# Optimization experiments

Measured on AMD Instinct MI355X. Metric: run time of the kernel, lower is better.

Reference implementation:

```python
import jax, jax.numpy as jnp
import numpy as np

N = 100000  # num nodes
E = 1600000  # num edges


def gcn_conv(x, edge_index, W, b):
    """PyG-style GCNConv: add self-loops, symmetric deg^-1/2 normalization,
    message = norm * (x @ W) gathered from src, scatter-add to dst, then + bias."""
    n = x.shape[0]
    loop = jnp.arange(n)
    src = jnp.concatenate([edge_index[0], loop])
    dst = jnp.concatenate([edge_index[1], loop])
    deg = jax.ops.segment_sum(jnp.ones_like(dst, dtype=x.dtype), dst, num_segments=n)
    dinv = jnp.where(deg > 0, jax.lax.rsqrt(deg), jnp.zeros_like(deg))
    norm = dinv[src] * dinv[dst]  # [E+N]
    h = x @ W  # dense transform first (out_dim <= in_dim here)
    msg = h[src] * norm[:, None]  # gather + scale, [E+N, out]
    out = jax.ops.segment_sum(msg, dst, num_segments=n)  # scatter-add
    return out + b


def setup_inputs() -> dict:
    key = jax.random.key(0)
    ks = jax.random.split(key, 6)
    x = jax.random.normal(ks[0], (N, 165), dtype=jnp.float32)
    edge_index = jax.random.randint(ks[1], (2, E), 0, N, dtype=jnp.int64)
    W1 = jax.random.normal(ks[2], (165, 128), dtype=jnp.float32) * 0.05
    b1 = jnp.zeros((128,), dtype=jnp.float32)
    W2 = jax.random.normal(ks[3], (128, 2), dtype=jnp.float32) * 0.05
    b2 = jnp.zeros((2,), dtype=jnp.float32)
    Ws = jax.random.normal(ks[4], (165, 2), dtype=jnp.float32) * 0.05
    bs = jnp.zeros((2,), dtype=jnp.float32)
    return {"x": x, "edge_index": edge_index, "W1": W1, "b1": b1,
            "W2": W2, "b2": b2, "Ws": Ws, "bs": bs}


def reference(x, edge_index, W1, b1, W2, b2, Ws, bs):
    h = jax.nn.relu(gcn_conv(x, edge_index, W1, b1))
    # dropout is identity at inference (training=False)
    out = gcn_conv(h, edge_index, W2, b2)
    return out + (x @ Ws + bs)
```

## Files before the change

kernel.cpp:

```cpp
#include <hip/hip_runtime.h>
#include <hip/hip_bf16.h>


#define IND 165
#define HID 128
#define KP 192
#define BM 32
#define XSS2 208
#define SLAB 8192
#define MAXNB 512

typedef __attribute__((ext_vector_type(8))) short short8v;
typedef __attribute__((ext_vector_type(4))) float float4v;
typedef __attribute__((ext_vector_type(2))) float float2v;

__device__ __forceinline__ unsigned short f2bf(float f) {
    unsigned u = __float_as_uint(f);
    unsigned r = (u + 0x7FFF + ((u >> 16) & 1)) >> 16;
    return (unsigned short)r;
}
__device__ __forceinline__ float bf2f(unsigned short s) { return __uint_as_float(((unsigned)s) << 16); }

__global__ __launch_bounds__(256) void setup_kernel(const float* __restrict__ W1,
                                                    unsigned short* __restrict__ w1t,
                                                    const int* __restrict__ e32,
                                                    int* __restrict__ flag,
                                                    int* __restrict__ bucket_len, int NB) {
    int b = blockIdx.x;
    if (b < 96) {
        int t = b * 256 + threadIdx.x;
        int nn = t / KP, k = t - nn * KP;
        w1t[t] = (k < IND) ? f2bf(W1[k * HID + nn]) : (unsigned short)0;
    } else {
        __shared__ int nz;
        if (threadIdx.x == 0) nz = 0;
        __syncthreads();
        if (e32[2 * threadIdx.x + 1] != 0) atomicOr(&nz, 1);
        __syncthreads();
        if (threadIdx.x == 0) flag[0] = (nz == 0) ? 1 : 0;
        for (int t = threadIdx.x; t < NB; t += 256) bucket_len[t] = 0;
    }
}

__global__ __launch_bounds__(256) void partition_kernel(const int* __restrict__ e32,
                                                        const int* __restrict__ flag,
                                                        int* __restrict__ bucket_len,
                                                        unsigned* __restrict__ slab,
                                                        int E, int NB) {
    __shared__ unsigned hist[MAXNB];
    __shared__ unsigned runbase[MAXNB];
    __shared__ unsigned cnt2[MAXNB];
    for (int t = threadIdx.x; t < NB; t += 256) { hist[t] = 0; cnt2[t] = 0; }
    __syncthreads();
    const int f = flag[0];
    const int base = blockIdx.x * 8192;
    unsigned rec[32];
    unsigned bk[32];
    #pragma unroll
    for (int j = 0; j < 32; ++j) {
        int e = base + j * 256 + threadIdx.x;
        if (e < E) {
            int src, dst;
            if (f) {
                int2 s2 = ((const int2*)e32)[e];
                int2 d2 = ((const int2*)e32)[E + e];
                src = s2.x; dst = d2.x;
            } else {
                src = e32[e];
                dst = e32[E + e];
            }
            unsigned b = (unsigned)dst >> 8;
            rec[j] = ((unsigned)(dst & 255) << 24) | (unsigned)src;
            bk[j] = b;
            atomicAdd(&hist[b], 1u);
        } else {
            bk[j] = 0xFFFFFFFFu;
            rec[j] = 0;
        }
    }
    __syncthreads();
    for (int t = threadIdx.x; t < NB; t += 256) {
        unsigned h = hist[t];
        runbase[t] = h ? (unsigned)atomicAdd(&bucket_len[t], (int)h) : 0u;
    }
    __syncthreads();
    #pragma unroll
    for (int j = 0; j < 32; ++j) {
        unsigned b = bk[j];
        if (b != 0xFFFFFFFFu) {
            unsigned p = runbase[b] + atomicAdd(&cnt2[b], 1u);
            if (p < SLAB) slab[(size_t)b * SLAB + p] = rec[j];
        }
    }
}

__global__ __launch_bounds__(256) void buildb_kernel(const unsigned* __restrict__ slab,
                                                     const int* __restrict__ bucket_len,
                                                     int2* __restrict__ row2,
                                                     float* __restrict__ dinv,
                                                     int* __restrict__ col_src, int n) {
    __shared__ unsigned deg[256];
    __shared__ int qa[256], qb[256];
    __shared__ unsigned cur[256];
    const int b = blockIdx.x;
    const int t = threadIdx.x;
    const int len = min(bucket_len[b], SLAB);
    const unsigned* recs = slab + (size_t)b * SLAB;
    const int d0 = b << 8;
    const int base = b * SLAB;
    deg[t] = 0;
    __syncthreads();
    for (int i = t; i < len; i += 256) atomicAdd(&deg[recs[i] >> 24], 1u);
    __syncthreads();
    const unsigned dv = deg[t];
    const int pdv = (int)((dv + 7u) & ~7u);
    qa[t] = pdv;
    __syncthreads();
    int* s = qa; int* d = qb;
    for (int off = 1; off < 256; off <<= 1) {
        d[t] = s[t] + ((t >= off) ? s[t - off] : 0);
        __syncthreads();
        int* tmp = s; s = d; d = tmp;
    }
    int pexcl = s[t] - pdv;
    int pend = min(pexcl + pdv, SLAB);
    if (pexcl > SLAB) pexcl = SLAB;
    if (d0 + t < n) {
        dinv[d0 + t] = rsqrtf(1.0f + (float)dv);
        row2[d0 + t] = make_int2(base + pexcl, base + pend);
    }
    cur[t] = (unsigned)pexcl;
    __syncthreads();
    for (int i = t; i < len; i += 256) {
        unsigned r = recs[i];
        unsigned p = atomicAdd(&cur[r >> 24], 1u);
        if (p < (unsigned)SLAB) col_src[base + p] = (int)(r & 0xFFFFFFu);
    }
    for (int p = pexcl + (int)dv; p < pend; ++p)
        col_src[base + p] = n;
}

__global__ __launch_bounds__(256, 4) void gemm1_kernel(const float* __restrict__ x,
                                                       const unsigned short* __restrict__ w1t,
                                                       const float* __restrict__ Ws,
                                                       const float* __restrict__ bs,
                                                       const float* __restrict__ b2,
                                                       const float* __restrict__ dinv,
                                                       unsigned char* __restrict__ hb8,
                                                       float* __restrict__ h2p,
                                                       float* __restrict__ skip, int n) {
    __shared__ unsigned short xs[BM * XSS2];
    __shared__ float sdinv[BM];
    const int row0 = blockIdx.x * BM;
    const int tid = threadIdx.x;
    const int wave = tid >> 6, lane = tid & 63;
    const int l15 = lane & 15, lk = (lane >> 4) * 8;

    if (blockIdx.x == 0) {
        if (tid < 32) ((unsigned*)(hb8 + (size_t)n * HID))[tid] = 0u;
        if (tid == 32) ((float2*)h2p)[n] = make_float2(0.f, 0.f);
    }
    if (tid < BM) sdinv[tid] = (row0 + tid < n) ? dinv[row0 + tid] : 1.f;

    short8v bfr[12];
    #pragma unroll
    for (int nt2 = 0; nt2 < 2; ++nt2)
        #pragma unroll
        for (int ks = 0; ks < 6; ++ks)
            bfr[nt2 * 6 + ks] =
                *(const short8v*)(w1t + (size_t)((2 * wave + nt2) * 16 + l15) * KP + ks * 32 + lk);

    for (int t = tid; t < BM * (XSS2 - IND); t += 256) {
        int r = t / (XSS2 - IND), k = IND + (t - r * (XSS2 - IND));
        xs[r * XSS2 + k] = 0;
    }
    {
        const int rows = min(BM, n - row0);
        const int nflt = rows * IND;
        const float2* xsrc = (const float2*)(x + (size_t)row0 * IND);
        const int nf2 = nflt >> 1;
        for (int f = tid; f < nf2; f += 256) {
            float2 v = xsrc[f];
            int e0 = 2 * f;
            int r0 = e0 / IND, k0 = e0 - r0 * IND;
            xs[r0 * XSS2 + k0] = f2bf(v.x);
            int r1 = (k0 == IND - 1) ? r0 + 1 : r0;
            int k1 = (k0 == IND - 1) ? 0 : k0 + 1;
            xs[r1 * XSS2 + k1] = f2bf(v.y);
        }
        if ((nflt & 1) && tid == 0) {
            int e = nflt - 1;
            int r = e / IND, k = e - r * IND;
            xs[r * XSS2 + k] = f2bf(x[(size_t)row0 * IND + e]);
        }
    }
    __syncthreads();

    float4v acc[2][2];
    #pragma unroll
    for (int m = 0; m < 2; ++m)
        #pragma unroll
        for (int nt2 = 0; nt2 < 2; ++nt2) acc[m][nt2] = (float4v){0.f, 0.f, 0.f, 0.f};
    #pragma unroll
    for (int m = 0; m < 2; ++m) {
        const unsigned short* arow = xs + (m * 16 + l15) * XSS2;
        #pragma unroll
        for (int ks = 0; ks < 6; ++ks) {
            short8v a = *(const short8v*)(arow + ks * 32 + lk);
            acc[m][0] = __builtin_amdgcn_mfma_f32_16x16x32_bf16(a, bfr[ks], acc[m][0], 0, 0, 0);
            acc[m][1] = __builtin_amdgcn_mfma_f32_16x16x32_bf16(a, bfr[6 + ks], acc[m][1], 0, 0, 0);
        }
    }

    #pragma unroll
    for (int m = 0; m < 2; ++m) {
        int rib0 = m * 16 + (lane >> 4) * 4;
        #pragma unroll
        for (int nt2 = 0; nt2 < 2; ++nt2) {
            int col = (2 * wave + nt2) * 16 + l15;
            #pragma unroll
            for (int r = 0; r < 4; ++r) {
                int row = row0 + rib0 + r;
                float hv = acc[m][nt2][r] * sdinv[rib0 + r];
                int pk = __builtin_amdgcn_cvt_pk_fp8_f32(hv, 0.f, 0, false);
                if (row < n) hb8[(size_t)row * HID + col] = (unsigned char)(pk & 0xFF);
            }
        }
    }

    {
        int r = tid >> 3, j = tid & 7;
        int row = row0 + r;
        float s0 = 0.f, s1 = 0.f;
        if (row < n) {
            const float2* Wsv = (const float2*)Ws;
            const unsigned short* xr = xs + r * XSS2;
            for (int k = j; k < IND; k += 8) {
                float xv = bf2f(xr[k]);
                float2 w = Wsv[k];
                s0 = fmaf(xv, w.x, s0);
                s1 = fmaf(xv, w.y, s1);
            }
        }
        s0 += __shfl_xor(s0, 1); s0 += __shfl_xor(s0, 2); s0 += __shfl_xor(s0, 4);
        s1 += __shfl_xor(s1, 1); s1 += __shfl_xor(s1, 2); s1 += __shfl_xor(s1, 4);
        if (j == 0 && row < n)
            ((float2*)skip)[row] = make_float2(s0 + bs[0] + b2[0], s1 + bs[1] + b2[1]);
    }
}

__global__ __launch_bounds__(256) void agg1_kernel(const unsigned char* __restrict__ hb8,
                                                   const float* __restrict__ dinv,
                                                   const int2* __restrict__ row2,
                                                   const int* __restrict__ col_src,
                                                   const float* __restrict__ b1,
                                                   const float* __restrict__ W2,
                                                   float* __restrict__ h2p, int n) {
    int wid = threadIdx.x >> 6, lane = threadIdx.x & 63;
    int i = blockIdx.x * 4 + wid;
    if (i >= n) return;
    const int slot = lane >> 4, cl = lane & 15;
    const float di = dinv[i];
    float2v a0, a1, a2, a3;
    {
        uint2 r = *(const uint2*)(hb8 + (size_t)i * 128 + cl * 8);
        float w = (slot == 0) ? 1.f : 0.f;
        float2v wv = {w, w};
        a0 = __builtin_amdgcn_cvt_pk_f32_fp8((int)r.x, false) * wv;
        a1 = __builtin_amdgcn_cvt_pk_f32_fp8((int)r.x, true)  * wv;
        a2 = __builtin_amdgcn_cvt_pk_f32_fp8((int)r.y, false) * wv;
        a3 = __builtin_amdgcn_cvt_pk_f32_fp8((int)r.y, true)  * wv;
    }
    const int2 be = row2[i];
    const int beg  = __builtin_amdgcn_readfirstlane(be.x);
    const int endv = __builtin_amdgcn_readfirstlane(be.y);
    for (int e = beg; e < endv; e += 8) {
        int4 c0 = *(const int4*)(col_src + e);
        int4 c1 = *(const int4*)(col_src + e + 4);
        int sx0 = (slot & 1) ? c0.y : c0.x;
        int sy0 = (slot & 1) ? c0.w : c0.z;
        int s0  = (slot & 2) ? sy0 : sx0;
        int sx1 = (slot & 1) ? c1.y : c1.x;
        int sy1 = (slot & 1) ? c1.w : c1.z;
        int s1  = (slot & 2) ? sy1 : sx1;
        uint2 r0 = *(const uint2*)(hb8 + (size_t)s0 * 128 + cl * 8);
        uint2 r1 = *(const uint2*)(hb8 + (size_t)s1 * 128 + cl * 8);
        a0 += __builtin_amdgcn_cvt_pk_f32_fp8((int)r0.x, false);
        a1 += __builtin_amdgcn_cvt_pk_f32_fp8((int)r0.x, true);
        a2 += __builtin_amdgcn_cvt_pk_f32_fp8((int)r0.y, false);
        a3 += __builtin_amdgcn_cvt_pk_f32_fp8((int)r0.y, true);
        a0 += __builtin_amdgcn_cvt_pk_f32_fp8((int)r1.x, false);
        a1 += __builtin_amdgcn_cvt_pk_f32_fp8((int)r1.x, true);
        a2 += __builtin_amdgcn_cvt_pk_f32_fp8((int)r1.y, false);
        a3 += __builtin_amdgcn_cvt_pk_f32_fp8((int)r1.y, true);
    }
    float a[8] = {a0.x, a0.y, a1.x, a1.y, a2.x, a2.y, a3.x, a3.y};
    #pragma unroll
    for (int c = 0; c < 8; ++c) {
        a[c] += __shfl_xor(a[c], 16);
        a[c] += __shfl_xor(a[c], 32);
    }
    float4 bA = ((const float4*)b1)[2 * cl];
    float4 bB = ((const float4*)b1)[2 * cl + 1];
    float v0 = fmaxf(fmaf(di, a[0], bA.x), 0.f);
    float v1 = fmaxf(fmaf(di, a[1], bA.y), 0.f);
    float v2 = fmaxf(fmaf(di, a[2], bA.z), 0.f);
    float v3 = fmaxf(fmaf(di, a[3], bA.w), 0.f);
    float v4 = fmaxf(fmaf(di, a[4], bB.x), 0.f);
    float v5 = fmaxf(fmaf(di, a[5], bB.y), 0.f);
    float v6 = fmaxf(fmaf(di, a[6], bB.z), 0.f);
    float v7 = fmaxf(fmaf(di, a[7], bB.w), 0.f);
    float4 wA = ((const float4*)W2)[4 * cl];
    float4 wB = ((const float4*)W2)[4 * cl + 1];
    float4 wC = ((const float4*)W2)[4 * cl + 2];
    float4 wD = ((const float4*)W2)[4 * cl + 3];
    float p0 = v0 * wA.x + v1 * wA.z + v2 * wB.x + v3 * wB.z
             + v4 * wC.x + v5 * wC.z + v6 * wD.x + v7 * wD.z;
    float p1 = v0 * wA.y + v1 * wA.w + v2 * wB.y + v3 * wB.w
             + v4 * wC.y + v5 * wC.w + v6 * wD.y + v7 * wD.w;
    p0 += __shfl_xor(p0, 1); p0 += __shfl_xor(p0, 2);
    p0 += __shfl_xor(p0, 4); p0 += __shfl_xor(p0, 8);
    p1 += __shfl_xor(p1, 1); p1 += __shfl_xor(p1, 2);
    p1 += __shfl_xor(p1, 4); p1 += __shfl_xor(p1, 8);
    if (lane == 0) ((float2*)h2p)[i] = make_float2(p0 * di, p1 * di);
}

__global__ __launch_bounds__(256) void agg2_kernel(const float* __restrict__ h2p,
                                                   const float* __restrict__ dinv,
                                                   const int2* __restrict__ row2,
                                                   const int* __restrict__ col_src,
                                                   const float* __restrict__ skip,
                                                   float* __restrict__ out, int n) {
    int wid = threadIdx.x >> 6, lane = threadIdx.x & 63;
    int i = blockIdx.x * 4 + wid;
    if (i >= n) return;
    float di = dinv[i];
    float a0 = 0.f, a1 = 0.f;
    const int2 be = row2[i];
    const int beg  = __builtin_amdgcn_readfirstlane(be.x);
    const int endv = __builtin_amdgcn_readfirstlane(be.y);
    for (int e = beg + lane; e < endv; e += 64) {
        int s = col_src[e];
        float2 hs = ((const float2*)h2p)[s];
        a0 += hs.x;
        a1 += hs.y;
    }
    #pragma unroll
    for (int off = 32; off; off >>= 1) {
        a0 += __shfl_xor(a0, off);
        a1 += __shfl_xor(a1, off);
    }
    if (lane == 0) {
        float2 self = ((const float2*)h2p)[i];
        float2 sk = ((const float2*)skip)[i];
        ((float2*)out)[i] = make_float2(di * (a0 + self.x) + sk.x,
                                        di * (a1 + self.y) + sk.y);
    }
}

extern "C" void kernel_launch(void* const* d_in, const int* in_sizes, int n_in,
                              void* d_out, int out_size, void* d_ws, size_t ws_size,
                              hipStream_t stream) {
    const float* x  = (const float*)d_in[0];
    const int*   ei = (const int*)d_in[1];
    const float* W1 = (const float*)d_in[2];
    const float* b1 = (const float*)d_in[3];
    const float* W2 = (const float*)d_in[4];
    const float* b2 = (const float*)d_in[5];
    const float* Ws = (const float*)d_in[6];
    const float* bs = (const float*)d_in[7];
    float* out = (float*)d_out;

    const int n = in_sizes[0] / IND;
    const int E = in_sizes[1] / 2;
    const int NB = (n + 255) >> 8;

    char* ws = (char*)d_ws;
    size_t off = 0;
    auto alloc = [&](size_t bytes) { void* p = ws + off; off += (bytes + 255) & ~(size_t)255; return p; };
    int*            flag        = (int*)alloc(256);
    int*            bucket_len  = (int*)alloc((size_t)(MAXNB + 1) * 4);
    unsigned*       slab        = (unsigned*)alloc((size_t)NB * SLAB * 4);
    int2*           row2        = (int2*)alloc((size_t)n * 8);
    float*          dinv        = (float*)alloc((size_t)n * 4);
    int*            col_src     = (int*)alloc((size_t)NB * SLAB * 4);
    unsigned char*  hb8         = (unsigned char*)alloc((size_t)(n + 1) * HID);
    float*          h2p         = (float*)alloc((size_t)(n + 1) * 2 * 4);
    float*          skip        = (float*)alloc((size_t)n * 2 * 4);
    unsigned short* w1t         = (unsigned short*)alloc((size_t)HID * KP * 2);
    (void)ws_size;

    setup_kernel<<<97, 256, 0, stream>>>(W1, w1t, ei, flag, bucket_len, NB);
    partition_kernel<<<(E + 8191) / 8192, 256, 0, stream>>>(ei, flag, bucket_len, slab, E, NB);
    buildb_kernel<<<NB, 256, 0, stream>>>(slab, bucket_len, row2, dinv, col_src, n);

    gemm1_kernel<<<(n + BM - 1) / BM, 256, 0, stream>>>(x, w1t, Ws, bs, b2, dinv, hb8, h2p, skip, n);
    agg1_kernel<<<(n + 3) / 4, 256, 0, stream>>>(hb8, dinv, row2, col_src, b1, W2, h2p, n);
    agg2_kernel<<<(n + 3) / 4, 256, 0, stream>>>(h2p, dinv, row2, col_src, skip, out, n);
}
```

Measured before the change: 167.5 us.

## Gather 16 edges per iteration with 16-byte fp8 row loads in agg1

```diff
diff --git a/kernel.cpp b/kernel.cpp
--- a/kernel.cpp
+++ b/kernel.cpp
@@ -20,6 +20,16 @@
     return (unsigned short)r;
 }
 __device__ __forceinline__ float bf2f(unsigned short s) { return __uint_as_float(((unsigned)s) << 16); }
+
+__device__ __forceinline__ int sel8(int4 a, int4 b, int slot) {
+    int t0 = (slot & 1) ? a.y : a.x;
+    int t1 = (slot & 1) ? a.w : a.z;
+    int t2 = (slot & 1) ? b.y : b.x;
+    int t3 = (slot & 1) ? b.w : b.z;
+    int u0 = (slot & 2) ? t1 : t0;
+    int u1 = (slot & 2) ? t3 : t2;
+    return (slot & 4) ? u1 : u0;
+}
 
 __global__ __launch_bounds__(256) void setup_kernel(const float* __restrict__ W1,
                                                     unsigned short* __restrict__ w1t,
@@ -113,7 +123,7 @@
     for (int i = t; i < len; i += 256) atomicAdd(&deg[recs[i] >> 24], 1u);
     __syncthreads();
     const unsigned dv = deg[t];
-    const int pdv = (int)((dv + 7u) & ~7u);
+    const int pdv = (int)((dv + 15u) & ~15u);
     qa[t] = pdv;
     __syncthreads();
     int* s = qa; int* d = qb;
@@ -259,69 +269,75 @@
     int wid = threadIdx.x >> 6, lane = threadIdx.x & 63;
     int i = blockIdx.x * 4 + wid;
     if (i >= n) return;
-    const int slot = lane >> 4, cl = lane & 15;
+    const int slot = lane >> 3, cb = lane & 7;
     const float di = dinv[i];
-    float2v a0, a1, a2, a3;
+    float2v a[8];
     {
-        uint2 r = *(const uint2*)(hb8 + (size_t)i * 128 + cl * 8);
+        uint4 r = *(const uint4*)(hb8 + (size_t)i * 128 + cb * 16);
         float w = (slot == 0) ? 1.f : 0.f;
         float2v wv = {w, w};
-        a0 = __builtin_amdgcn_cvt_pk_f32_fp8((int)r.x, false) * wv;
-        a1 = __builtin_amdgcn_cvt_pk_f32_fp8((int)r.x, true)  * wv;
-        a2 = __builtin_amdgcn_cvt_pk_f32_fp8((int)r.y, false) * wv;
-        a3 = __builtin_amdgcn_cvt_pk_f32_fp8((int)r.y, true)  * wv;
+        a[0] = __builtin_amdgcn_cvt_pk_f32_fp8((int)r.x, false) * wv;
+        a[1] = __builtin_amdgcn_cvt_pk_f32_fp8((int)r.x, true)  * wv;
+        a[2] = __builtin_amdgcn_cvt_pk_f32_fp8((int)r.y, false) * wv;
+        a[3] = __builtin_amdgcn_cvt_pk_f32_fp8((int)r.y, true)  * wv;
+        a[4] = __builtin_amdgcn_cvt_pk_f32_fp8((int)r.z, false) * wv;
+        a[5] = __builtin_amdgcn_cvt_pk_f32_fp8((int)r.z, true)  * wv;
+        a[6] = __builtin_amdgcn_cvt_pk_f32_fp8((int)r.w, false) * wv;
+        a[7] = __builtin_amdgcn_cvt_pk_f32_fp8((int)r.w, true)  * wv;
     }
     const int2 be = row2[i];
     const int beg  = __builtin_amdgcn_readfirstlane(be.x);
     const int endv = __builtin_amdgcn_readfirstlane(be.y);
-    for (int e = beg; e < endv; e += 8) {
-        int4 c0 = *(const int4*)(col_src + e);
-        int4 c1 = *(const int4*)(col_src + e + 4);
-        int sx0 = (slot & 1) ? c0.y : c0.x;
-        int sy0 = (slot & 1) ? c0.w : c0.z;
-        int s0  = (slot & 2) ? sy0 : sx0;
-        int sx1 = (slot & 1) ? c1.y : c1.x;
-        int sy1 = (slot & 1) ? c1.w : c1.z;
-        int s1  = (slot & 2) ? sy1 : sx1;
-        uint2 r0 = *(const uint2*)(hb8 + (size_t)s0 * 128 + cl * 8);
-        uint2 r1 = *(const uint2*)(hb8 + (size_t)s1 * 128 + cl * 8);
-        a0 += __builtin_amdgcn_cvt_pk_f32_fp8((int)r0.x, false);
-        a1 += __builtin_amdgcn_cvt_pk_f32_fp8((int)r0.x, true);
-        a2 += __builtin_amdgcn_cvt_pk_f32_fp8((int)r0.y, false);
-        a3 += __builtin_amdgcn_cvt_pk_f32_fp8((int)r0.y, true);
-        a0 += __builtin_amdgcn_cvt_pk_f32_fp8((int)r1.x, false);
-        a1 += __builtin_amdgcn_cvt_pk_f32_fp8((int)r1.x, true);
-        a2 += __builtin_amdgcn_cvt_pk_f32_fp8((int)r1.y, false);
-        a3 += __builtin_amdgcn_cvt_pk_f32_fp8((int)r1.y, true);
-    }
-    float a[8] = {a0.x, a0.y, a1.x, a1.y, a2.x, a2.y, a3.x, a3.y};
-    #pragma unroll
-    for (int c = 0; c < 8; ++c) {
-        a[c] += __shfl_xor(a[c], 16);
-        a[c] += __shfl_xor(a[c], 32);
-    }
-    float4 bA = ((const float4*)b1)[2 * cl];
-    float4 bB = ((const float4*)b1)[2 * cl + 1];
-    float v0 = fmaxf(fmaf(di, a[0], bA.x), 0.f);
-    float v1 = fmaxf(fmaf(di, a[1], bA.y), 0.f);
-    float v2 = fmaxf(fmaf(di, a[2], bA.z), 0.f);
-    float v3 = fmaxf(fmaf(di, a[3], bA.w), 0.f);
-    float v4 = fmaxf(fmaf(di, a[4], bB.x), 0.f);
-    float v5 = fmaxf(fmaf(di, a[5], bB.y), 0.f);
-    float v6 = fmaxf(fmaf(di, a[6], bB.z), 0.f);
-    float v7 = fmaxf(fmaf(di, a[7], bB.w), 0.f);
-    float4 wA = ((const float4*)W2)[4 * cl];
-    float4 wB = ((const float4*)W2)[4 * cl + 1];
-    float4 wC = ((const float4*)W2)[4 * cl + 2];
-    float4 wD = ((const float4*)W2)[4 * cl + 3];
-    float p0 = v0 * wA.x + v1 * wA.z + v2 * wB.x + v3 * wB.z
-             + v4 * wC.x + v5 * wC.z + v6 * wD.x + v7 * wD.z;
-    float p1 = v0 * wA.y + v1 * wA.w + v2 * wB.y + v3 * wB.w
-             + v4 * wC.y + v5 * wC.w + v6 * wD.y + v7 * wD.w;
-    p0 += __shfl_xor(p0, 1); p0 += __shfl_xor(p0, 2);
-    p0 += __shfl_xor(p0, 4); p0 += __shfl_xor(p0, 8);
-    p1 += __shfl_xor(p1, 1); p1 += __shfl_xor(p1, 2);
-    p1 += __shfl_xor(p1, 4); p1 += __shfl_xor(p1, 8);
+    for (int e = beg; e < endv; e += 16) {
+        int4 ca = *(const int4*)(col_src + e);
+        int4 cbv = *(const int4*)(col_src + e + 4);
+        int4 cc = *(const int4*)(col_src + e + 8);
+        int4 cd = *(const int4*)(col_src + e + 12);
+        int s0 = sel8(ca, cbv, slot);
+        int s1 = sel8(cc, cd, slot);
+        uint4 r0 = *(const uint4*)(hb8 + (size_t)s0 * 128 + cb * 16);
+        uint4 r1 = *(const uint4*)(hb8 + (size_t)s1 * 128 + cb * 16);
+        a[0] += __builtin_amdgcn_cvt_pk_f32_fp8((int)r0.x, false);
+        a[1] += __builtin_amdgcn_cvt_pk_f32_fp8((int)r0.x, true);
+        a[2] += __builtin_amdgcn_cvt_pk_f32_fp8((int)r0.y, false);
+        a[3] += __builtin_amdgcn_cvt_pk_f32_fp8((int)r0.y, true);
+        a[4] += __builtin_amdgcn_cvt_pk_f32_fp8((int)r0.z, false);
+        a[5] += __builtin_amdgcn_cvt_pk_f32_fp8((int)r0.z, true);
+        a[6] += __builtin_amdgcn_cvt_pk_f32_fp8((int)r0.w, false);
+        a[7] += __builtin_amdgcn_cvt_pk_f32_fp8((int)r0.w, true);
+        a[0] += __builtin_amdgcn_cvt_pk_f32_fp8((int)r1.x, false);
+        a[1] += __builtin_amdgcn_cvt_pk_f32_fp8((int)r1.x, true);
+        a[2] += __builtin_amdgcn_cvt_pk_f32_fp8((int)r1.y, false);
+        a[3] += __builtin_amdgcn_cvt_pk_f32_fp8((int)r1.y, true);
+        a[4] += __builtin_amdgcn_cvt_pk_f32_fp8((int)r1.z, false);
+        a[5] += __builtin_amdgcn_cvt_pk_f32_fp8((int)r1.z, true);
+        a[6] += __builtin_amdgcn_cvt_pk_f32_fp8((int)r1.w, false);
+        a[7] += __builtin_amdgcn_cvt_pk_f32_fp8((int)r1.w, true);
+    }
+    float f[16];
+    #pragma unroll
+    for (int c = 0; c < 8; ++c) { f[2 * c] = a[c].x; f[2 * c + 1] = a[c].y; }
+    #pragma unroll
+    for (int c = 0; c < 16; ++c) {
+        f[c] += __shfl_xor(f[c], 8);
+        f[c] += __shfl_xor(f[c], 16);
+        f[c] += __shfl_xor(f[c], 32);
+    }
+    float p0 = 0.f, p1 = 0.f;
+    #pragma unroll
+    for (int q = 0; q < 4; ++q) {
+        float4 bb = ((const float4*)b1)[4 * cb + q];
+        float4 wa = ((const float4*)W2)[8 * cb + 2 * q];
+        float4 wb = ((const float4*)W2)[8 * cb + 2 * q + 1];
+        float v0 = fmaxf(fmaf(di, f[4 * q + 0], bb.x), 0.f);
+        float v1 = fmaxf(fmaf(di, f[4 * q + 1], bb.y), 0.f);
+        float v2 = fmaxf(fmaf(di, f[4 * q + 2], bb.z), 0.f);
+        float v3 = fmaxf(fmaf(di, f[4 * q + 3], bb.w), 0.f);
+        p0 += v0 * wa.x + v1 * wa.z + v2 * wb.x + v3 * wb.z;
+        p1 += v0 * wa.y + v1 * wa.w + v2 * wb.y + v3 * wb.w;
+    }
+    p0 += __shfl_xor(p0, 1); p0 += __shfl_xor(p0, 2); p0 += __shfl_xor(p0, 4);
+    p1 += __shfl_xor(p1, 1); p1 += __shfl_xor(p1, 2); p1 += __shfl_xor(p1, 4);
     if (lane == 0) ((float2*)h2p)[i] = make_float2(p0 * di, p1 * di);
 }
 
```

Result: slower. 238.6 us (+42.4%).
